# Optimization experiments

Hardware: AMD Instinct MI355X
Metric: run time of the kernel (lower is better)

The kernel has to match this reference:

```python
import jax, jax.numpy as jnp
import numpy as np
from jax import lax

B, IN_CH, OUT_CH, H, W = 32, 128, 256, 64, 64
STYLE_CH, TDIM, G = 512, 512, 32
GN_EPS, MOD_EPS = 1e-5, 1e-8
DN = ('NCHW', 'OIHW', 'NCHW')


def swish(x):
    return x * jax.nn.sigmoid(x)


def group_norm(x, gamma, beta):
    n, c, h, w = x.shape
    xr = x.reshape(n, G, c // G, h, w)
    mu = xr.mean(axis=(2, 3, 4), keepdims=True)
    var = xr.var(axis=(2, 3, 4), keepdims=True)
    xn = ((xr - mu) * lax.rsqrt(var + GN_EPS)).reshape(n, c, h, w)
    return xn * gamma[None, :, None, None] + beta[None, :, None, None]


def conv3x3(x, w, b):
    y = lax.conv_general_dilated(x, w, (1, 1), ((1, 1), (1, 1)), dimension_numbers=DN)
    return y + b[None, :, None, None]


def setup_inputs() -> dict:
    key = jax.random.key(0)
    ks = jax.random.split(key, 16)
    s = 0.05
    return {
        'x': jax.random.normal(ks[0], (B, IN_CH, H, W), jnp.float32),
        'temb': jax.random.normal(ks[1], (B, TDIM), jnp.float32),
        'style': jax.random.normal(ks[2], (B, STYLE_CH), jnp.float32),
        'gn1_g': jnp.ones((IN_CH,), jnp.float32),
        'gn1_b': jnp.zeros((IN_CH,), jnp.float32),
        'conv1_w': jax.random.normal(ks[3], (OUT_CH, IN_CH, 3, 3), jnp.float32) * s,
        'conv1_b': jnp.zeros((OUT_CH,), jnp.float32),
        'temb_w': jax.random.normal(ks[4], (OUT_CH, TDIM), jnp.float32) * s,
        'temb_b': jnp.zeros((OUT_CH,), jnp.float32),
        'gn2_g': jnp.ones((OUT_CH,), jnp.float32),
        'gn2_b': jnp.zeros((OUT_CH,), jnp.float32),
        'style_w': jax.random.normal(ks[5], (OUT_CH, STYLE_CH), jnp.float32) * s,
        'style_b': jnp.zeros((OUT_CH,), jnp.float32),
        'mod_w': jax.random.normal(ks[6], (OUT_CH, OUT_CH, 3, 3), jnp.float32) * s,
        'sc_w': jax.random.normal(ks[7], (OUT_CH, IN_CH, 1, 1), jnp.float32) * s,
        'sc_b': jnp.zeros((OUT_CH,), jnp.float32),
    }


def reference(x, temb, style, gn1_g, gn1_b, conv1_w, conv1_b, temb_w, temb_b,
              gn2_g, gn2_b, style_w, style_b, mod_w, sc_w, sc_b):
    # block1: GN -> Swish -> Conv3x3
    h = conv3x3(swish(group_norm(x, gn1_g, gn1_b)), conv1_w, conv1_b)
    # temb projection: Swish -> Linear, broadcast over HxW
    h = h + (swish(temb) @ temb_w.T + temb_b)[:, :, None, None]
    # block2: GN -> Swish -> Dropout(0) [identity]
    h = swish(group_norm(h, gn2_g, gn2_b))
    # modulated + demodulated per-sample conv (StyleGAN2-style)
    style2 = style @ style_w.T + style_b                       # (b, out_ch)
    wmod = mod_w[None] * (style2[:, None, :, None, None] + 1.0)  # (b, o, i, kh, kw)
    d = lax.rsqrt((wmod ** 2).sum(axis=(2, 3, 4), keepdims=True) + MOD_EPS)
    wmod = wmod * d
    conv1s = lambda xi, wi: lax.conv_general_dilated(
        xi[None], wi, (1, 1), ((1, 1), (1, 1)), dimension_numbers=DN)[0]
    h = jax.vmap(conv1s)(h, wmod)                              # per-sample conv
    # shortcut 1x1 conv (in_ch != out_ch)
    sc = lax.conv_general_dilated(x, sc_w, (1, 1), ((0, 0), (0, 0)), dimension_numbers=DN)
    sc = sc + sc_b[None, :, None, None]
    return h + sc
```

## Files before the change

### kernel.cpp

```cpp
#include <hip/hip_runtime.h>
#include <cstdint>

typedef unsigned short u16;
typedef unsigned int   u32;

typedef __attribute__((ext_vector_type(8))) short bf16x8;
typedef __attribute__((ext_vector_type(4))) float f32x4;

#define DEV __device__ __forceinline__

static constexpr int HP = 66, WP = 66;

DEV u16 f2bf(float f) {
  u32 u = __float_as_uint(f);
  u32 r = (u + 0x7fffu + ((u >> 16) & 1u)) >> 16;
  return (u16)r;
}
DEV float bf2f(u16 v) { return __uint_as_float((u32)v << 16); }

DEV void gload_lds16(const void* g, void* s) {
  __builtin_amdgcn_global_load_lds(
      (const __attribute__((address_space(1))) void*)g,
      (__attribute__((address_space(3))) void*)s, 16, 0, 0);
}

__global__ __launch_bounds__(256) void repack_w_kernel(const float* __restrict__ src,
                                                       u16* __restrict__ dst,
                                                       int Cin, int K, int total,
                                                       int ksq, int kdim) {
  for (int idx = blockIdx.x * 256 + threadIdx.x; idx < total; idx += gridDim.x * 256) {
    int co = idx / K;
    int r  = idx - co * K;
    int s  = r / Cin;
    int ci = r - s * Cin;
    int ky = s / kdim, kx = s - ky * kdim;
    dst[idx] = f2bf(src[(co * Cin + ci) * ksq + ky * kdim + kx]);
  }
}

__global__ __launch_bounds__(256) void modw_ss_kernel(const float* __restrict__ w,
                                                      float* __restrict__ SS_T) {
  int o = blockIdx.x, i = threadIdx.x;
  const float* p = w + (size_t)(o * 256 + i) * 9;
  float s = 0.f;
#pragma unroll
  for (int k = 0; k < 9; ++k) s += p[k] * p[k];
  SS_T[i * 256 + o] = s;
}

__global__ __launch_bounds__(256) void style_mvec_kernel(const float* __restrict__ style,
                                                         const float* __restrict__ style_w,
                                                         const float* __restrict__ style_b,
                                                         float* __restrict__ mvec) {
  __shared__ float st[512];
  int b = blockIdx.x, t = threadIdx.x;
  for (int k = t; k < 512; k += 256) st[k] = style[b * 512 + k];
  __syncthreads();
  const float4* wr = (const float4*)(style_w + t * 512);
  float acc = 0.f;
  for (int k = 0; k < 128; ++k) {
    float4 w4 = wr[k];
    acc += w4.x * st[k*4] + w4.y * st[k*4+1] + w4.z * st[k*4+2] + w4.w * st[k*4+3];
  }
  mvec[b * 256 + t] = acc + style_b[t] + 1.f;
}

__global__ __launch_bounds__(256) void demod_kernel(const float* __restrict__ mvec,
                                                    const float* __restrict__ SS_T,
                                                    float* __restrict__ dvec) {
  __shared__ float m2[256];
  int b = blockIdx.x, t = threadIdx.x;
  float mv = mvec[b * 256 + t];
  m2[t] = mv * mv;
  __syncthreads();
  float acc = 0.f;
  for (int i = 0; i < 256; ++i) acc += m2[i] * SS_T[i * 256 + t];
  dvec[b * 256 + t] = rsqrtf(acc + 1e-8f);
}

__global__ __launch_bounds__(256) void scale_sc_kernel(const float* __restrict__ sc_w,
                                                       const float* __restrict__ dvec,
                                                       u16* __restrict__ scTb) {
  int idx = blockIdx.x * 256 + threadIdx.x;
  int ci = idx & 127;
  int co = (idx >> 7) & 255;
  int b  = idx >> 15;
  scTb[idx] = f2bf(sc_w[co * 128 + ci] / dvec[b * 256 + co]);
}

__global__ __launch_bounds__(256) void temb_proj_kernel(const float* __restrict__ temb,
                                                        const float* __restrict__ temb_w,
                                                        const float* __restrict__ temb_b,
                                                        const float* __restrict__ conv1_b,
                                                        float* __restrict__ tb2) {
  __shared__ float sw[512];
  int b = blockIdx.x, t = threadIdx.x;
  for (int k = t; k < 512; k += 256) {
    float v = temb[b * 512 + k];
    sw[k] = v / (1.f + __expf(-v));
  }
  __syncthreads();
  const float4* wr = (const float4*)(temb_w + t * 512);
  float acc = 0.f;
  for (int k = 0; k < 128; ++k) {
    float4 w4 = wr[k];
    acc += w4.x * sw[k*4] + w4.y * sw[k*4+1] + w4.z * sw[k*4+2] + w4.w * sw[k*4+3];
  }
  tb2[b * 256 + t] = acc + temb_b[t] + conv1_b[t];
}

template <int C>
__global__ __launch_bounds__(256) void halo_zero_kernel(u16* __restrict__ buf) {
  int idx = blockIdx.x * 256 + threadIdx.x;
  const int GR = C / 8;
  if (idx >= 32 * 260 * GR) return;
  int g = idx % GR;
  int p = (idx / GR) % 260;
  int b = idx / (GR * 260);
  int y, x;
  if (p < 66)       { y = 0;        x = p; }
  else if (p < 132) { y = 65;       x = p - 66; }
  else if (p < 196) { y = p - 131;  x = 0; }
  else              { y = p - 195;  x = 65; }
  uint4 z; z.x = 0; z.y = 0; z.z = 0; z.w = 0;
  *(uint4*)(buf + (((size_t)b * HP + y) * WP + x) * C + g * 8) = z;
}

__global__ __launch_bounds__(256) void gn1_stats_kernel(const float* __restrict__ x,
                                                        float2* __restrict__ st1) {
  int bg = blockIdx.x;
  const float4* p = (const float4*)(x + (size_t)bg * 16384);
  float s = 0.f, s2 = 0.f;
  for (int i = threadIdx.x; i < 4096; i += 256) {
    float4 v = p[i];
    s  += v.x + v.y + v.z + v.w;
    s2 += v.x*v.x + v.y*v.y + v.z*v.z + v.w*v.w;
  }
  for (int d = 32; d; d >>= 1) { s += __shfl_down(s, d); s2 += __shfl_down(s2, d); }
  __shared__ float red[2][4];
  if ((threadIdx.x & 63) == 0) { red[0][threadIdx.x >> 6] = s; red[1][threadIdx.x >> 6] = s2; }
  __syncthreads();
  if (threadIdx.x == 0) {
    s  = red[0][0] + red[0][1] + red[0][2] + red[0][3];
    s2 = red[1][0] + red[1][1] + red[1][2] + red[1][3];
    float mean = s / 16384.f;
    float var  = s2 / 16384.f - mean * mean;
    st1[bg] = make_float2(mean, rsqrtf(var + 1e-5f));
  }
}

__global__ __launch_bounds__(256) void gn1_apply_kernel(const float* __restrict__ x,
                                                        const float2* __restrict__ st1,
                                                        const float* __restrict__ g1,
                                                        const float* __restrict__ b1,
                                                        u16* __restrict__ act1p,
                                                        u16* __restrict__ xh) {
  __shared__ float xs[128][65];
  int blk = blockIdx.x;
  int b = blk >> 6, y = blk & 63;
  int t = threadIdx.x;
#pragma unroll 8
  for (int pass = 0; pass < 32; ++pass) {
    int c = pass * 4 + (t >> 6);
    xs[c][t & 63] = x[(((size_t)b * 128 + c) * 64 + y) * 64 + (t & 63)];
  }
  __syncthreads();
  for (int pass = 0; pass < 32; ++pass) {
    int xc = pass * 2 + (t >> 7);
    int c  = t & 127;
    float v = xs[c][xc];
    float2 ms = st1[b * 32 + (c >> 2)];
    float vn = (v - ms.x) * ms.y * g1[c] + b1[c];
    float sw = vn / (1.f + __expf(-vn));
    act1p[(((size_t)b * HP + (y + 1)) * WP + (xc + 1)) * 128 + c] = f2bf(sw);
    xh[(((size_t)b * 64 + y) * 64 + xc) * 128 + c] = f2bf(v);
  }
}

__global__ void gn2_final_kernel(const float* __restrict__ st2sum, float2* __restrict__ st2) {
  int idx = blockIdx.x * 256 + threadIdx.x;
  if (idx >= 1024) return;
  float s  = st2sum[idx * 2];
  float s2 = st2sum[idx * 2 + 1];
  float mean = s / 32768.f;
  float var  = s2 / 32768.f - mean * mean;
  st2[idx] = make_float2(mean, rsqrtf(var + 1e-5f));
}

__global__ __launch_bounds__(256) void gn2_apply_kernel(const u16* __restrict__ h1,
                                                        const float2* __restrict__ st2,
                                                        const float* __restrict__ g2,
                                                        const float* __restrict__ b2,
                                                        const float* __restrict__ mvec,
                                                        u16* __restrict__ act2p) {
  int idx = blockIdx.x * 256 + threadIdx.x;
  int gpix = idx >> 5;
  int gi = idx & 31;
  int c0 = gi * 8;
  int b = gpix >> 12, y = (gpix >> 6) & 63, x = gpix & 63;
  uint4 raw = *(const uint4*)(h1 + (size_t)gpix * 256 + c0);
  const u16* rs = (const u16*)&raw;
  float2 ms = st2[b * 32 + gi];
  const float* mv = mvec + b * 256 + c0;
  u16 outp[8];
#pragma unroll
  for (int e = 0; e < 8; ++e) {
    float v  = bf2f(rs[e]);
    float vn = (v - ms.x) * ms.y * g2[c0 + e] + b2[c0 + e];
    float sw = vn / (1.f + __expf(-vn));
    outp[e] = f2bf(sw * mv[e]);
  }
  *(uint4*)(act2p + (((size_t)b * HP + (y + 1)) * WP + (x + 1)) * 256 + c0) = *(const uint4*)outp;
}

template <int MODE>
__global__ __launch_bounds__(512, 2) void igemm_kernel(const u16* __restrict__ act,
                                                       const u16* __restrict__ wT,
                                                       const float* __restrict__ epi,
                                                       const u16* __restrict__ xh,
                                                       const u16* __restrict__ scTb,
                                                       const float* __restrict__ sc_b,
                                                       u16* __restrict__ h1out,
                                                       float* __restrict__ fout,
                                                       float* __restrict__ st2sum) {
  constexpr int CIN    = (MODE == 0) ? 128 : 256;
  constexpr int NSUB   = CIN / 64;
  constexpr int KW     = CIN * 9;
  constexpr int NKMAIN = KW / 64;
  constexpr int NKT    = (MODE == 2) ? NKMAIN + 2 : NKMAIN;

  __shared__ __align__(16) unsigned char lds[131072];
  const int tid  = threadIdx.x;
  const int wave = tid >> 6, lane = tid & 63;
  const int wm = wave >> 2, wn = wave & 3;
  const int m_base = blockIdx.x * 256;
  const int bimg = m_base >> 12;
  const int ln = lane & 15, l4 = lane >> 4;

  const int srow = lane >> 3;
  const int glog = (lane & 7) ^ srow;

  u32 pixA[2][2], pixX[2][2], rowB[2][2], rowS[2][2];
#pragma unroll
  for (int j = 0; j < 2; ++j)
#pragma unroll
    for (int h = 0; h < 2; ++h) {
      int mlocal = (wave & 3) * 16 + j * 8 + srow + h * 64 + (wave >> 2) * 128;
      int m = m_base + mlocal;
      int y = (m >> 6) & 63, x = m & 63;
      pixA[j][h] = (u32)((bimg * HP + y) * WP + x) * CIN + glog * 8;
      if (MODE == 2) pixX[j][h] = (u32)m * 128 + glog * 8;
      int co = (wave >> 1) * 64 + h * 32 + (wave & 1) * 16 + j * 8 + srow;
      rowB[j][h] = (u32)co * KW + glog * 8;
      if (MODE == 2) rowS[j][h] = (u32)(bimg * 256 + co) * 128 + glog * 8;
    }

  f32x4 acc[8][4];
#pragma unroll
  for (int i = 0; i < 8; ++i)
#pragma unroll
    for (int j = 0; j < 4; ++j) acc[i][j] = (f32x4){0.f, 0.f, 0.f, 0.f};

  auto stageA = [&](int kt, int h, int buf) {
    unsigned char* dst = lds + buf * 65536 + h * 16384 + wave * 2048;
    if (MODE == 2 && kt >= NKMAIN) {
      u32 ko = (u32)(kt - NKMAIN) * 64;
      gload_lds16(xh + pixX[0][h] + ko, dst);
      gload_lds16(xh + pixX[1][h] + ko, dst + 1024);
    } else {
      int tap = kt / NSUB;
      int kin = (kt - tap * NSUB) * 64;
      int ky = tap / 3, kx = tap - ky * 3;
      u32 ko = (u32)((ky * WP + kx) * CIN + kin);
      gload_lds16(act + pixA[0][h] + ko, dst);
      gload_lds16(act + pixA[1][h] + ko, dst + 1024);
    }
  };
  auto stageB = [&](int kt, int g, int buf) {
    unsigned char* dst = lds + buf * 65536 + 32768 + g * 16384 + wave * 2048;
    if (MODE == 2 && kt >= NKMAIN) {
      u32 ko = (u32)(kt - NKMAIN) * 64;
      gload_lds16(scTb + rowS[0][g] + ko, dst);
      gload_lds16(scTb + rowS[1][g] + ko, dst + 1024);
    } else {
      u32 ko = (u32)kt * 64;
      gload_lds16(wT + rowB[0][g] + ko, dst);
      gload_lds16(wT + rowB[1][g] + ko, dst + 1024);
    }
  };

  bf16x8 af[8], bf[4];
  auto ldA = [&](int h, int buf) {
    const unsigned char* As = lds + buf * 65536;
#pragma unroll
    for (int f = 0; f < 4; ++f)
#pragma unroll
      for (int kk = 0; kk < 2; ++kk) {
        int lr = h * 128 + wm * 64 + f * 16 + ln;
        int gr = (kk * 4 + l4) ^ (ln & 7);
        af[f * 2 + kk] = *(const bf16x8*)(As + lr * 128 + gr * 16);
      }
  };
  auto ldB = [&](int g, int buf) {
    const unsigned char* Bs = lds + buf * 65536 + 32768;
#pragma unroll
    for (int f1 = 0; f1 < 2; ++f1)
#pragma unroll
      for (int kk = 0; kk < 2; ++kk) {
        int lr = g * 128 + wn * 32 + f1 * 16 + ln;
        int gr = (kk * 4 + l4) ^ (ln & 7);
        bf[f1 * 2 + kk] = *(const bf16x8*)(Bs + lr * 128 + gr * 16);
      }
  };
  auto mmac = [&](int h, int g) {
    __builtin_amdgcn_s_setprio(1);
#pragma unroll
    for (int f = 0; f < 4; ++f)
#pragma unroll
      for (int f1 = 0; f1 < 2; ++f1)
#pragma unroll
        for (int kk = 0; kk < 2; ++kk)
          acc[h * 4 + f][g * 2 + f1] = __builtin_amdgcn_mfma_f32_16x16x32_bf16(
              af[f * 2 + kk], bf[f1 * 2 + kk], acc[h * 4 + f][g * 2 + f1], 0, 0, 0);
    __builtin_amdgcn_s_setprio(0);
  };

#define PHASE_BAR() do { __builtin_amdgcn_sched_barrier(0); \
    __builtin_amdgcn_s_barrier(); __builtin_amdgcn_sched_barrier(0); } while (0)

  stageA(0, 0, 0); stageB(0, 0, 0); stageB(0, 1, 0); stageA(0, 1, 0);

#pragma unroll 2
  for (int kt = 0; kt < NKT - 1; ++kt) {
    const int cur = kt & 1, nxt = cur ^ 1;
    stageA(kt + 1, 0, nxt);
    asm volatile("s_waitcnt vmcnt(6)" ::: "memory");
    PHASE_BAR();
    ldB(0, cur); ldA(0, cur);
    mmac(0, 0);
    stageB(kt + 1, 0, nxt);
    asm volatile("s_waitcnt vmcnt(6)" ::: "memory");
    PHASE_BAR();
    ldB(1, cur);
    mmac(0, 1);
    stageB(kt + 1, 1, nxt);
    asm volatile("s_waitcnt vmcnt(6)" ::: "memory");
    PHASE_BAR();
    ldA(1, cur);
    mmac(1, 1);
    stageA(kt + 1, 1, nxt);
    PHASE_BAR();
    ldB(0, cur);
    mmac(1, 0);
  }
  {
    const int cur = (NKT - 1) & 1;
    asm volatile("s_waitcnt vmcnt(4)" ::: "memory");
    PHASE_BAR();
    ldB(0, cur); ldA(0, cur); mmac(0, 0);
    asm volatile("s_waitcnt vmcnt(2)" ::: "memory");
    PHASE_BAR();
    ldB(1, cur); mmac(0, 1);
    asm volatile("s_waitcnt vmcnt(0)" ::: "memory");
    PHASE_BAR();
    ldA(1, cur); mmac(1, 1);
    PHASE_BAR();
    ldB(0, cur); mmac(1, 0);
  }
#undef PHASE_BAR

  if (MODE == 0) {
    const float* tbrow = epi + bimg * 256;
    float ps[4], ps2[4];
#pragma unroll
    for (int fn = 0; fn < 4; ++fn) { ps[fn] = 0.f; ps2[fn] = 0.f; }
#pragma unroll
    for (int fm = 0; fm < 8; ++fm)
#pragma unroll
      for (int fn = 0; fn < 4; ++fn) {
        int co = wn * 64 + fn * 16 + ln;
        float add = tbrow[co];
#pragma unroll
        for (int i = 0; i < 4; ++i) {
          int m = m_base + wm * 128 + fm * 16 + (l4 << 2) + i;
          float v = acc[fm][fn][i] + add;
          h1out[(size_t)m * 256 + co] = f2bf(v);
          ps[fn] += v; ps2[fn] += v * v;
        }
      }
#pragma unroll
    for (int fn = 0; fn < 4; ++fn) {
      float s = ps[fn], s2 = ps2[fn];
      s += __shfl_xor(s, 1);  s2 += __shfl_xor(s2, 1);
      s += __shfl_xor(s, 2);  s2 += __shfl_xor(s2, 2);
      s += __shfl_xor(s, 4);  s2 += __shfl_xor(s2, 4);
      s += __shfl_xor(s, 16); s2 += __shfl_xor(s2, 16);
      s += __shfl_xor(s, 32); s2 += __shfl_xor(s2, 32);
      if ((lane & 55) == 0) {
        int g = wn * 8 + fn * 2 + (ln >> 3);
        atomicAdd(&st2sum[bimg * 64 + g * 2 + 0], s);
        atomicAdd(&st2sum[bimg * 64 + g * 2 + 1], s2);
      }
    }
  } else {
    float* tile = (float*)lds;
    const int pixb = m_base & 4095;
#pragma unroll
    for (int c = 0; c < 4; ++c) {
      __syncthreads();
      if (wn == c) {
#pragma unroll
        for (int fn = 0; fn < 4; ++fn) {
          int nl = fn * 16 + ln;
          int co = c * 64 + nl;
          float dsc = epi[bimg * 256 + co];
          float scb = sc_b[co];
#pragma unroll
          for (int fm = 0; fm < 8; ++fm)
#pragma unroll
            for (int i = 0; i < 4; ++i) {
              int ml = wm * 128 + fm * 16 + (l4 << 2) + i;
              tile[nl * 257 + ml] = acc[fm][fn][i] * dsc + scb;
            }
        }
      }
      __syncthreads();
#pragma unroll 4
      for (int it = 0; it < 32; ++it) {
        int lin = it * 512 + tid;
        int co_l = lin >> 8, ml = lin & 255;
        fout[((size_t)(bimg * 256 + c * 64 + co_l)) * 4096 + pixb + ml] =
            tile[co_l * 257 + ml];
      }
    }
  }
}

extern "C" void kernel_launch(void* const* d_in, const int* in_sizes, int n_in,
                              void* d_out, int out_size, void* d_ws, size_t ws_size,
                              hipStream_t stream) {
  const float* x       = (const float*)d_in[0];
  const float* temb    = (const float*)d_in[1];
  const float* style   = (const float*)d_in[2];
  const float* gn1_g   = (const float*)d_in[3];
  const float* gn1_b   = (const float*)d_in[4];
  const float* conv1_w = (const float*)d_in[5];
  const float* conv1_b = (const float*)d_in[6];
  const float* temb_w  = (const float*)d_in[7];
  const float* temb_b  = (const float*)d_in[8];
  const float* gn2_g   = (const float*)d_in[9];
  const float* gn2_b   = (const float*)d_in[10];
  const float* style_w = (const float*)d_in[11];
  const float* style_b = (const float*)d_in[12];
  const float* mod_w   = (const float*)d_in[13];
  const float* sc_w    = (const float*)d_in[14];
  const float* sc_b    = (const float*)d_in[15];
  float* out = (float*)d_out;
  char* ws = (char*)d_ws;

  size_t o = 0;
  auto alloc = [&](size_t bytes) { size_t r = o; o += (bytes + 255) & ~(size_t)255; return r; };
  const size_t act1p_bytes = (size_t)32 * HP * WP * 128 * 2;
  const size_t xh_bytes    = (size_t)32 * 64 * 64 * 128 * 2;
  const size_t h1_bytes    = (size_t)32 * 4096 * 256 * 2;
  const size_t act2p_bytes = (size_t)32 * HP * WP * 256 * 2;
  size_t o_act1p = alloc(act1p_bytes);
  size_t o_xh    = alloc(xh_bytes);
  size_t o_h1    = alloc(h1_bytes);
  size_t o_act2p = alloc(act2p_bytes);
  size_t o_w1T   = alloc((size_t)256 * 1152 * 2);
  size_t o_wmT   = alloc((size_t)256 * 2304 * 2);
  size_t o_scTb  = alloc((size_t)32 * 256 * 128 * 2);
  size_t o_tb2   = alloc(8192 * 4);
  size_t o_mvec  = alloc(8192 * 4);
  size_t o_dvec  = alloc(8192 * 4);
  size_t o_SS    = alloc((size_t)256 * 256 * 4);
  size_t o_st1   = alloc(1024 * 8);
  size_t o_st2   = alloc(1024 * 8);
  size_t o_s2sum = alloc(32 * 32 * 2 * 4);
  if (ws_size < o) return;

  u16*    act1p = (u16*)(ws + o_act1p);
  u16*    xh    = (u16*)(ws + o_xh);
  u16*    h1    = (u16*)(ws + o_h1);
  u16*    act2p = (u16*)(ws + o_act2p);
  u16*    w1T   = (u16*)(ws + o_w1T);
  u16*    wmT   = (u16*)(ws + o_wmT);
  u16*    scTb  = (u16*)(ws + o_scTb);
  float*  tb2   = (float*)(ws + o_tb2);
  float*  mvec  = (float*)(ws + o_mvec);
  float*  dvec  = (float*)(ws + o_dvec);
  float*  SS_T  = (float*)(ws + o_SS);
  float2* st1   = (float2*)(ws + o_st1);
  float2* st2   = (float2*)(ws + o_st2);
  float*  s2sum = (float*)(ws + o_s2sum);

  halo_zero_kernel<128><<<(32 * 260 * 16 + 255) / 256, 256, 0, stream>>>(act1p);
  halo_zero_kernel<256><<<(32 * 260 * 32 + 255) / 256, 256, 0, stream>>>(act2p);
  hipMemsetAsync(s2sum, 0, 32 * 32 * 2 * 4, stream);

  repack_w_kernel<<<1152, 256, 0, stream>>>(conv1_w, w1T, 128, 1152, 256 * 1152, 9, 3);
  repack_w_kernel<<<2304, 256, 0, stream>>>(mod_w, wmT, 256, 2304, 256 * 2304, 9, 3);
  modw_ss_kernel<<<256, 256, 0, stream>>>(mod_w, SS_T);
  temb_proj_kernel<<<32, 256, 0, stream>>>(temb, temb_w, temb_b, conv1_b, tb2);
  style_mvec_kernel<<<32, 256, 0, stream>>>(style, style_w, style_b, mvec);
  demod_kernel<<<32, 256, 0, stream>>>(mvec, SS_T, dvec);
  scale_sc_kernel<<<4096, 256, 0, stream>>>(sc_w, dvec, scTb);
  gn1_stats_kernel<<<1024, 256, 0, stream>>>(x, st1);
  gn1_apply_kernel<<<2048, 256, 0, stream>>>(x, st1, gn1_g, gn1_b, act1p, xh);

  igemm_kernel<0><<<512, 512, 0, stream>>>(act1p, w1T, tb2, nullptr, nullptr,
                                           nullptr, h1, nullptr, s2sum);

  gn2_final_kernel<<<4, 256, 0, stream>>>(s2sum, st2);
  gn2_apply_kernel<<<16384, 256, 0, stream>>>(h1, st2, gn2_g, gn2_b, mvec, act2p);

  igemm_kernel<2><<<512, 512, 0, stream>>>(act2p, wmT, dvec, xh, scTb,
                                           sc_b, nullptr, out, nullptr);
}
```

Baseline: 375.0 us.

## Merge prep kernels, fold GN2 finalize, and vectorize GN1 apply stores

```diff
diff --git a/kernel.cpp b/kernel.cpp
--- a/kernel.cpp
+++ b/kernel.cpp
@@ -24,45 +24,95 @@
       (__attribute__((address_space(3))) void*)s, 16, 0, 0);
 }
 
-__global__ __launch_bounds__(256) void repack_w_kernel(const float* __restrict__ src,
-                                                       u16* __restrict__ dst,
-                                                       int Cin, int K, int total,
-                                                       int ksq, int kdim) {
-  for (int idx = blockIdx.x * 256 + threadIdx.x; idx < total; idx += gridDim.x * 256) {
-    int co = idx / K;
-    int r  = idx - co * K;
-    int s  = r / Cin;
-    int ci = r - s * Cin;
-    int ky = s / kdim, kx = s - ky * kdim;
-    dst[idx] = f2bf(src[(co * Cin + ci) * ksq + ky * kdim + kx]);
-  }
-}
-
-__global__ __launch_bounds__(256) void modw_ss_kernel(const float* __restrict__ w,
-                                                      float* __restrict__ SS_T) {
-  int o = blockIdx.x, i = threadIdx.x;
-  const float* p = w + (size_t)(o * 256 + i) * 9;
-  float s = 0.f;
-#pragma unroll
-  for (int k = 0; k < 9; ++k) s += p[k] * p[k];
-  SS_T[i * 256 + o] = s;
-}
-
-__global__ __launch_bounds__(256) void style_mvec_kernel(const float* __restrict__ style,
+__global__ __launch_bounds__(256) void prep_kernel(const float* __restrict__ conv1_w,
+                                                   const float* __restrict__ mod_w,
+                                                   u16* __restrict__ w1T,
+                                                   u16* __restrict__ wmT,
+                                                   float* __restrict__ SS_T,
+                                                   u16* __restrict__ act1p,
+                                                   u16* __restrict__ act2p,
+                                                   float* __restrict__ s2sum) {
+  int blk = blockIdx.x, t = threadIdx.x;
+  if (blk < 1152) {
+    int idx = blk * 256 + t;
+    int co = idx / 1152, r = idx - co * 1152;
+    int s = r >> 7, ci = r & 127;
+    int ky = s / 3, kx = s - ky * 3;
+    w1T[idx] = f2bf(conv1_w[(co * 128 + ci) * 9 + ky * 3 + kx]);
+  } else if (blk < 3456) {
+    int idx = (blk - 1152) * 256 + t;
+    int co = idx / 2304, r = idx - co * 2304;
+    int s = r >> 8, ci = r & 255;
+    int ky = s / 3, kx = s - ky * 3;
+    wmT[idx] = f2bf(mod_w[(co * 256 + ci) * 9 + ky * 3 + kx]);
+  } else if (blk < 3712) {
+    int o = blk - 3456, i = t;
+    const float* p = mod_w + (size_t)(o * 256 + i) * 9;
+    float s = 0.f;
+#pragma unroll
+    for (int k = 0; k < 9; ++k) s += p[k] * p[k];
+    SS_T[i * 256 + o] = s;
+  } else if (blk < 5272) {
+    bool big = blk >= 4232;
+    int idx = (big ? (blk - 4232) : (blk - 3712)) * 256 + t;
+    const int GR = big ? 32 : 16;
+    int g = idx % GR;
+    int p = (idx / GR) % 260;
+    int b = idx / (GR * 260);
+    int y, x;
+    if (p < 66)       { y = 0;       x = p; }
+    else if (p < 132) { y = 65;      x = p - 66; }
+    else if (p < 196) { y = p - 131; x = 0; }
+    else              { y = p - 195; x = 65; }
+    uint4 z; z.x = 0; z.y = 0; z.z = 0; z.w = 0;
+    u16* buf = big ? act2p : act1p;
+    int C = big ? 256 : 128;
+    *(uint4*)(buf + (((size_t)b * HP + y) * WP + x) * C + g * 8) = z;
+  } else {
+    *(float2*)(s2sum + t * 8)     = make_float2(0.f, 0.f);
+    *(float2*)(s2sum + t * 8 + 2) = make_float2(0.f, 0.f);
+    *(float2*)(s2sum + t * 8 + 4) = make_float2(0.f, 0.f);
+    *(float2*)(s2sum + t * 8 + 6) = make_float2(0.f, 0.f);
+  }
+}
+
+__global__ __launch_bounds__(256) void temb_style_kernel(const float* __restrict__ temb,
+                                                         const float* __restrict__ temb_w,
+                                                         const float* __restrict__ temb_b,
+                                                         const float* __restrict__ conv1_b,
+                                                         const float* __restrict__ style,
                                                          const float* __restrict__ style_w,
                                                          const float* __restrict__ style_b,
+                                                         float* __restrict__ tb2,
                                                          float* __restrict__ mvec) {
-  __shared__ float st[512];
-  int b = blockIdx.x, t = threadIdx.x;
-  for (int k = t; k < 512; k += 256) st[k] = style[b * 512 + k];
-  __syncthreads();
-  const float4* wr = (const float4*)(style_w + t * 512);
-  float acc = 0.f;
-  for (int k = 0; k < 128; ++k) {
-    float4 w4 = wr[k];
-    acc += w4.x * st[k*4] + w4.y * st[k*4+1] + w4.z * st[k*4+2] + w4.w * st[k*4+3];
-  }
-  mvec[b * 256 + t] = acc + style_b[t] + 1.f;
+  __shared__ float sw[512];
+  int blk = blockIdx.x, t = threadIdx.x;
+  if (blk < 32) {
+    int b = blk;
+    for (int k = t; k < 512; k += 256) {
+      float v = temb[b * 512 + k];
+      sw[k] = v / (1.f + __expf(-v));
+    }
+    __syncthreads();
+    const float4* wr = (const float4*)(temb_w + t * 512);
+    float acc = 0.f;
+    for (int k = 0; k < 128; ++k) {
+      float4 w4 = wr[k];
+      acc += w4.x * sw[k*4] + w4.y * sw[k*4+1] + w4.z * sw[k*4+2] + w4.w * sw[k*4+3];
+    }
+    tb2[b * 256 + t] = acc + temb_b[t] + conv1_b[t];
+  } else {
+    int b = blk - 32;
+    for (int k = t; k < 512; k += 256) sw[k] = style[b * 512 + k];
+    __syncthreads();
+    const float4* wr = (const float4*)(style_w + t * 512);
+    float acc = 0.f;
+    for (int k = 0; k < 128; ++k) {
+      float4 w4 = wr[k];
+      acc += w4.x * sw[k*4] + w4.y * sw[k*4+1] + w4.z * sw[k*4+2] + w4.w * sw[k*4+3];
+    }
+    mvec[b * 256 + t] = acc + style_b[t] + 1.f;
+  }
 }
 
 __global__ __launch_bounds__(256) void demod_kernel(const float* __restrict__ mvec,
@@ -88,44 +138,6 @@
   scTb[idx] = f2bf(sc_w[co * 128 + ci] / dvec[b * 256 + co]);
 }
 
-__global__ __launch_bounds__(256) void temb_proj_kernel(const float* __restrict__ temb,
-                                                        const float* __restrict__ temb_w,
-                                                        const float* __restrict__ temb_b,
-                                                        const float* __restrict__ conv1_b,
-                                                        float* __restrict__ tb2) {
-  __shared__ float sw[512];
-  int b = blockIdx.x, t = threadIdx.x;
-  for (int k = t; k < 512; k += 256) {
-    float v = temb[b * 512 + k];
-    sw[k] = v / (1.f + __expf(-v));
-  }
-  __syncthreads();
-  const float4* wr = (const float4*)(temb_w + t * 512);
-  float acc = 0.f;
-  for (int k = 0; k < 128; ++k) {
-    float4 w4 = wr[k];
-    acc += w4.x * sw[k*4] + w4.y * sw[k*4+1] + w4.z * sw[k*4+2] + w4.w * sw[k*4+3];
-  }
-  tb2[b * 256 + t] = acc + temb_b[t] + conv1_b[t];
-}
-
-template <int C>
-__global__ __launch_bounds__(256) void halo_zero_kernel(u16* __restrict__ buf) {
-  int idx = blockIdx.x * 256 + threadIdx.x;
-  const int GR = C / 8;
-  if (idx >= 32 * 260 * GR) return;
-  int g = idx % GR;
-  int p = (idx / GR) % 260;
-  int b = idx / (GR * 260);
-  int y, x;
-  if (p < 66)       { y = 0;        x = p; }
-  else if (p < 132) { y = 65;       x = p - 66; }
-  else if (p < 196) { y = p - 131;  x = 0; }
-  else              { y = p - 195;  x = 65; }
-  uint4 z; z.x = 0; z.y = 0; z.z = 0; z.w = 0;
-  *(uint4*)(buf + (((size_t)b * HP + y) * WP + x) * C + g * 8) = z;
-}
-
 __global__ __launch_bounds__(256) void gn1_stats_kernel(const float* __restrict__ x,
                                                         float2* __restrict__ st1) {
   int bg = blockIdx.x;
@@ -155,40 +167,43 @@
                                                         const float* __restrict__ b1,
                                                         u16* __restrict__ act1p,
                                                         u16* __restrict__ xh) {
-  __shared__ float xs[128][65];
+  __shared__ float xs[64][129];
   int blk = blockIdx.x;
   int b = blk >> 6, y = blk & 63;
   int t = threadIdx.x;
 #pragma unroll 8
   for (int pass = 0; pass < 32; ++pass) {
     int c = pass * 4 + (t >> 6);
-    xs[c][t & 63] = x[(((size_t)b * 128 + c) * 64 + y) * 64 + (t & 63)];
+    xs[t & 63][c] = x[(((size_t)b * 128 + c) * 64 + y) * 64 + (t & 63)];
   }
   __syncthreads();
-  for (int pass = 0; pass < 32; ++pass) {
-    int xc = pass * 2 + (t >> 7);
-    int c  = t & 127;
-    float v = xs[c][xc];
-    float2 ms = st1[b * 32 + (c >> 2)];
-    float vn = (v - ms.x) * ms.y * g1[c] + b1[c];
-    float sw = vn / (1.f + __expf(-vn));
-    act1p[(((size_t)b * HP + (y + 1)) * WP + (xc + 1)) * 128 + c] = f2bf(sw);
-    xh[(((size_t)b * 64 + y) * 64 + xc) * 128 + c] = f2bf(v);
-  }
-}
-
-__global__ void gn2_final_kernel(const float* __restrict__ st2sum, float2* __restrict__ st2) {
-  int idx = blockIdx.x * 256 + threadIdx.x;
-  if (idx >= 1024) return;
-  float s  = st2sum[idx * 2];
-  float s2 = st2sum[idx * 2 + 1];
-  float mean = s / 32768.f;
-  float var  = s2 / 32768.f - mean * mean;
-  st2[idx] = make_float2(mean, rsqrtf(var + 1e-5f));
+  const int cg = t & 15, c0 = cg * 8;
+  float2 msA = st1[b * 32 + cg * 2];
+  float2 msB = st1[b * 32 + cg * 2 + 1];
+  float g1r[8], b1r[8];
+#pragma unroll
+  for (int e = 0; e < 8; ++e) { g1r[e] = g1[c0 + e]; b1r[e] = b1[c0 + e]; }
+#pragma unroll
+  for (int p = 0; p < 4; ++p) {
+    int xi = p * 16 + (t >> 4);
+    u16 outA[8], outX[8];
+#pragma unroll
+    for (int e = 0; e < 8; ++e) {
+      float v = xs[xi][c0 + e];
+      float2 ms = (e < 4) ? msA : msB;
+      float vn = (v - ms.x) * ms.y * g1r[e] + b1r[e];
+      float sw = vn / (1.f + __expf(-vn));
+      outA[e] = f2bf(sw);
+      outX[e] = f2bf(v);
+    }
+    *(uint4*)(act1p + (((size_t)b * HP + (y + 1)) * WP + (xi + 1)) * 128 + c0) =
+        *(const uint4*)outA;
+    *(uint4*)(xh + (((size_t)b * 64 + y) * 64 + xi) * 128 + c0) = *(const uint4*)outX;
+  }
 }
 
 __global__ __launch_bounds__(256) void gn2_apply_kernel(const u16* __restrict__ h1,
-                                                        const float2* __restrict__ st2,
+                                                        const float* __restrict__ st2sum,
                                                         const float* __restrict__ g2,
                                                         const float* __restrict__ b2,
                                                         const float* __restrict__ mvec,
@@ -200,13 +215,16 @@
   int b = gpix >> 12, y = (gpix >> 6) & 63, x = gpix & 63;
   uint4 raw = *(const uint4*)(h1 + (size_t)gpix * 256 + c0);
   const u16* rs = (const u16*)&raw;
-  float2 ms = st2[b * 32 + gi];
+  float s  = st2sum[b * 64 + gi * 2];
+  float s2 = st2sum[b * 64 + gi * 2 + 1];
+  float mean = s / 32768.f;
+  float rstd = rsqrtf(s2 / 32768.f - mean * mean + 1e-5f);
   const float* mv = mvec + b * 256 + c0;
   u16 outp[8];
 #pragma unroll
   for (int e = 0; e < 8; ++e) {
     float v  = bf2f(rs[e]);
-    float vn = (v - ms.x) * ms.y * g2[c0 + e] + b2[c0 + e];
+    float vn = (v - mean) * rstd * g2[c0 + e] + b2[c0 + e];
     float sw = vn / (1.f + __expf(-vn));
     outp[e] = f2bf(sw * mv[e]);
   }
@@ -297,7 +315,7 @@
 #pragma unroll
       for (int kk = 0; kk < 2; ++kk) {
         int lr = h * 128 + wm * 64 + f * 16 + ln;
-        int gr = (kk * 4 + l4) ^ (ln & 7);
+        int gr = (kk * 4 + l4) ^ (lr & 7);
         af[f * 2 + kk] = *(const bf16x8*)(As + lr * 128 + gr * 16);
       }
   };
@@ -308,7 +326,7 @@
 #pragma unroll
       for (int kk = 0; kk < 2; ++kk) {
         int lr = g * 128 + wn * 32 + f1 * 16 + ln;
-        int gr = (kk * 4 + l4) ^ (ln & 7);
+        int gr = (kk * 4 + l4) ^ (lr & 7);
         bf[f1 * 2 + kk] = *(const bf16x8*)(Bs + lr * 128 + gr * 16);
       }
   };
@@ -476,7 +494,6 @@
   size_t o_dvec  = alloc(8192 * 4);
   size_t o_SS    = alloc((size_t)256 * 256 * 4);
   size_t o_st1   = alloc(1024 * 8);
-  size_t o_st2   = alloc(1024 * 8);
   size_t o_s2sum = alloc(32 * 32 * 2 * 4);
   if (ws_size < o) return;
 
@@ -492,28 +509,21 @@
   float*  dvec  = (float*)(ws + o_dvec);
   float*  SS_T  = (float*)(ws + o_SS);
   float2* st1   = (float2*)(ws + o_st1);
-  float2* st2   = (float2*)(ws + o_st2);
   float*  s2sum = (float*)(ws + o_s2sum);
 
-  halo_zero_kernel<128><<<(32 * 260 * 16 + 255) / 256, 256, 0, stream>>>(act1p);
-  halo_zero_kernel<256><<<(32 * 260 * 32 + 255) / 256, 256, 0, stream>>>(act2p);
-  hipMemsetAsync(s2sum, 0, 32 * 32 * 2 * 4, stream);
-
-  repack_w_kernel<<<1152, 256, 0, stream>>>(conv1_w, w1T, 128, 1152, 256 * 1152, 9, 3);
-  repack_w_kernel<<<2304, 256, 0, stream>>>(mod_w, wmT, 256, 2304, 256 * 2304, 9, 3);
-  modw_ss_kernel<<<256, 256, 0, stream>>>(mod_w, SS_T);
-  temb_proj_kernel<<<32, 256, 0, stream>>>(temb, temb_w, temb_b, conv1_b, tb2);
-  style_mvec_kernel<<<32, 256, 0, stream>>>(style, style_w, style_b, mvec);
+  prep_kernel<<<5273, 256, 0, stream>>>(conv1_w, mod_w, w1T, wmT, SS_T,
+                                        act1p, act2p, s2sum);
+  temb_style_kernel<<<64, 256, 0, stream>>>(temb, temb_w, temb_b, conv1_b,
+                                            style, style_w, style_b, tb2, mvec);
+  gn1_stats_kernel<<<1024, 256, 0, stream>>>(x, st1);
+  gn1_apply_kernel<<<2048, 256, 0, stream>>>(x, st1, gn1_g, gn1_b, act1p, xh);
   demod_kernel<<<32, 256, 0, stream>>>(mvec, SS_T, dvec);
   scale_sc_kernel<<<4096, 256, 0, stream>>>(sc_w, dvec, scTb);
-  gn1_stats_kernel<<<1024, 256, 0, stream>>>(x, st1);
-  gn1_apply_kernel<<<2048, 256, 0, stream>>>(x, st1, gn1_g, gn1_b, act1p, xh);
 
   igemm_kernel<0><<<512, 512, 0, stream>>>(act1p, w1T, tb2, nullptr, nullptr,
                                            nullptr, h1, nullptr, s2sum);
 
-  gn2_final_kernel<<<4, 256, 0, stream>>>(s2sum, st2);
-  gn2_apply_kernel<<<16384, 256, 0, stream>>>(h1, st2, gn2_g, gn2_b, mvec, act2p);
+  gn2_apply_kernel<<<16384, 256, 0, stream>>>(h1, s2sum, gn2_g, gn2_b, mvec, act2p);
 
   igemm_kernel<2><<<512, 512, 0, stream>>>(act2p, wmT, dvec, xh, scTb,
                                            sc_b, nullptr, out, nullptr);
```

Measured after the change: 340.7 us. 9.2% less time.
